# Optimization experiments

Hardware: AMD Instinct MI355X
Metric: run time of the kernel (lower is better)

The kernel has to match this reference:

```python
import jax, jax.numpy as jnp
import numpy as np

LN_EPS = 1e-3  # keras LayerNormalization default epsilon


def _prefix_weights(S, dtype):
    # W[i, j] = 1/(i-j)^2 for j < i, else 0  (distance = i - j)
    idx = jnp.arange(S)
    diff = idx[:, None] - idx[None, :]
    safe = jnp.where(diff > 0, diff, 1).astype(dtype)
    return jnp.where(diff > 0, 1.0 / (safe * safe), jnp.zeros((), dtype))


def setup_inputs() -> dict:
    key = jax.random.key(0)
    k1, k2 = jax.random.split(key)
    B, S, E = 2, 512, 256
    x = jax.random.normal(k1, (B, S, E), dtype=jnp.float32)
    concept_map = jax.random.normal(k2, (E, E, E), dtype=jnp.float32) * 0.02
    gamma = jnp.ones((E,), dtype=jnp.float32)
    beta = jnp.zeros((E,), dtype=jnp.float32)
    return {"x": x, "concept_map": concept_map, "gamma": gamma, "beta": beta}


def reference(x, concept_map, gamma, beta):
    B, S, E = x.shape
    # positional-weighted prefix sum: s[b,i,:] = sum_{j<i} x[b,j,:] / (i-j)^2
    W = _prefix_weights(S, x.dtype)            # (S, S) lower-triangular
    s = jnp.einsum('ij,bjd->bid', W, x)        # (B, S, E)
    # outer product x_i (x) s_i contracted with cubic concept_map:
    # result[b,i,c] = sum_{a,p} x[b,i,a] * s[b,i,p] * concept_map[c,a,p]
    # (stacked conceptual_matrices broadcast against concept_map, summed over
    #  the last two axes -- equivalent bilinear contraction)
    y = jnp.einsum('bsa,bsp,cap->bsc', x, s, concept_map)
    y = y + x  # residual
    # LayerNormalization over last axis (keras defaults: eps=1e-3, affine)
    mean = jnp.mean(y, axis=-1, keepdims=True)
    var = jnp.mean(jnp.square(y - mean), axis=-1, keepdims=True)
    y = (y - mean) * jax.lax.rsqrt(var + LN_EPS) * gamma + beta
    # Dropout is identity at inference
    return y
```

## Files before the change

### kernel.cpp

```cpp
#include <hip/hip_runtime.h>
#include <hip/hip_fp16.h>
#include <cstdint>

#define BB 2
#define SS 512
#define EE 256
#define NN (BB*SS)
#define KTOT (EE*EE)
#define SPLITK 32
#define KCHUNK (KTOT/SPLITK)
#define NSTEP (KCHUNK/32)
#define TSTEPS (KTOT/32)
#define LN_EPS 1e-3f

typedef _Float16 f16;
typedef _Float16 f16x8 __attribute__((ext_vector_type(8)));
typedef float    f32x4 __attribute__((ext_vector_type(4)));

#define NPACK 512

__global__ void prep_kernel(const float* __restrict__ cm, f16* __restrict__ cmP,
                            const float* __restrict__ x, float* __restrict__ ps) {
    __shared__ __align__(16) char smem[35072];
    const int bid = blockIdx.x;
    const int tid = threadIdx.x;
    const int wave = tid >> 6;
    const int lane = tid & 63;

    if (bid < NPACK) {
        const int cg = bid >> 7;
        const int kg = bid & 127;
        f16* lt = (f16*)smem;
        #pragma unroll
        for (int h = 0; h < 2; ++h) {
            #pragma unroll
            for (int i = 0; i < 8; ++i) {
                const int rl = i * 4 + wave;
                const int row = cg * 64 + h * 32 + rl;
                const float* src = cm + (size_t)row * KTOT + kg * 512 + lane * 8;
                float4 lo = *(const float4*)(src);
                float4 hi = *(const float4*)(src + 4);
                f16x8 v = { (f16)lo.x, (f16)lo.y, (f16)lo.z, (f16)lo.w,
                            (f16)hi.x, (f16)hi.y, (f16)hi.z, (f16)hi.w };
                *(f16x8*)(lt + lane * 264 + rl * 8) = v;
            }
            __syncthreads();
            #pragma unroll
            for (int jj = 0; jj < 8; ++jj) {
                const int s  = jj * 8 + wave * 2 + (lane >> 5);
                const int cl = lane & 31;
                f16x8 v = *(const f16x8*)(lt + s * 264 + cl * 8);
                const int t    = kg * 16 + (s >> 2);
                const int koct = s & 3;
                const int c    = cg * 64 + h * 32 + cl;
                *(f16x8*)(cmP + (size_t)t * 8192 + koct * 2048 + c * 8) = v;
            }
            __syncthreads();
        }
        return;
    }

    float (*xt)[128] = (float(*)[128])smem;
    float* wl2 = (float*)(smem + 32768);
    const int id = bid - NPACK;
    const int eh = id & 1;
    const int rest = id >> 1;
    const int b = rest / 36;
    const int r = rest % 36;
    int it = 0;
    while ((it + 1) * (it + 2) / 2 <= r) ++it;
    const int jt = r - it * (it + 1) / 2;

    for (int t = tid; t < 576; t += 256) {
        const int d = t - 64;
        wl2[t] = (d > 0) ? 1.0f / ((float)d * (float)d) : 0.0f;
    }
    const int jbase = jt * 64, ibase = it * 64;
    const float* xb = x + ((size_t)b * SS + jbase) * EE + eh * 128;
    #pragma unroll
    for (int p = 0; p < 8; ++p) {
        const int row = p * 8 + (tid >> 5);
        const int col = (tid & 31) * 4;
        *(float4*)&xt[row][col] = *(const float4*)(xb + (size_t)row * EE + col);
    }
    __syncthreads();

    const int g  = tid >> 5;
    const int ec = (tid & 31) * 4;
    const int irow = ibase + g * 8;
    float4 acc[8];
    #pragma unroll
    for (int m = 0; m < 8; ++m) acc[m] = (float4){0.f, 0.f, 0.f, 0.f};

    for (int jj = 0; jj < 64; ++jj) {
        const float4 xv = *(const float4*)&xt[jj][ec];
        const int wbase = irow - (jbase + jj) + 64;
        #pragma unroll
        for (int m = 0; m < 8; ++m) {
            const float w = wl2[wbase + m];
            acc[m].x += xv.x * w;
            acc[m].y += xv.y * w;
            acc[m].z += xv.z * w;
            acc[m].w += xv.w * w;
        }
    }

    float* base = ps + ((size_t)(((b * 2 + eh) * 8 + it) * 8 + jt)) * (64 * 128);
    #pragma unroll
    for (int m = 0; m < 8; ++m)
        *(float4*)(base + (size_t)(g * 8 + m) * 128 + ec) = acc[m];
}

__global__ void reduce_s_kernel(const float* __restrict__ ps, float* __restrict__ s) {
    const int n = blockIdx.x;
    const int e = threadIdx.x;
    const int b = n >> 9, i = n & (SS - 1);
    const int it = i >> 6, il = i & 63;
    const int eh = e >> 7, ec = e & 127;
    const size_t tbase = (size_t)((b * 2 + eh) * 8 + it) * 8;
    float acc = 0.0f;
    for (int jt = 0; jt <= it; ++jt)
        acc += ps[(tbase + jt) * (64 * 128) + (size_t)il * 128 + ec];
    s[(size_t)n * EE + e] = acc;
}

__launch_bounds__(256, 2)
__global__ void gemm_kernel(const float* __restrict__ x,
                            const float* __restrict__ sbuf,
                            const f16* __restrict__ cmP,
                            f16* __restrict__ part) {
    __shared__ __align__(16) f16 Ep[64 * 264];
    const int tid  = threadIdx.x;
    const int lane = tid & 63;
    const int wave = tid >> 6;
    const int koct = lane >> 4;
    const int cl   = lane & 15;

    const int d = blockIdx.x;
    const int nblock = (d >> 3) & 15;
    const int chunk  = (d & 7) * 4 + (d >> 7);

    f16x8 xf[4];
    #pragma unroll
    for (int rt = 0; rt < 4; ++rt) {
        const int r = nblock * 64 + rt * 16 + cl;
        const float* xr = x + (size_t)r * EE + chunk * 8;
        float4 xlo = *(const float4*)(xr);
        float4 xhi = *(const float4*)(xr + 4);
        xf[rt] = (f16x8){ (f16)xlo.x, (f16)xlo.y, (f16)xlo.z, (f16)xlo.w,
                          (f16)xhi.x, (f16)xhi.y, (f16)xhi.z, (f16)xhi.w };
    }
    float4 p0[4][2];
    #pragma unroll
    for (int rt = 0; rt < 4; ++rt) {
        const int r = nblock * 64 + rt * 16 + cl;
        const float* sr = sbuf + (size_t)r * EE + koct * 8;
        p0[rt][0] = *(const float4*)(sr);
        p0[rt][1] = *(const float4*)(sr + 4);
    }

    const char* bbase = (const char*)cmP + (size_t)chunk * (64 * 16384)
                      + koct * 4096 + wave * 1024 + cl * 16;
    #define TOFF(v) ((size_t)((((v) & 7) << 3) | ((v) >> 3)) * 16384)
    #define LOADB(BUF, v) do {                                              \
        _Pragma("unroll")                                                   \
        for (int ct_ = 0; ct_ < 4; ++ct_)                                   \
            BUF[ct_] = *(const f16x8*)(bbase + TOFF(v) + ct_ * 256);        \
    } while (0)

    f16x8 b0[4], b1[4], b2[4], b3[4];
    LOADB(b0, 0); LOADB(b1, 1); LOADB(b2, 2);
    __builtin_amdgcn_sched_barrier(0);

    f32x4 acc[4][4];
    #pragma unroll
    for (int a = 0; a < 4; ++a)
        #pragma unroll
        for (int b = 0; b < 4; ++b) acc[a][b] = (f32x4){0.f, 0.f, 0.f, 0.f};

    f16x8 svm[4];
    #pragma unroll
    for (int rt = 0; rt < 4; ++rt)
        svm[rt] = (f16x8){ (f16)p0[rt][0].x, (f16)p0[rt][0].y,
                           (f16)p0[rt][0].z, (f16)p0[rt][0].w,
                           (f16)p0[rt][1].x, (f16)p0[rt][1].y,
                           (f16)p0[rt][1].z, (f16)p0[rt][1].w };

    float4 pnxt[4][2];

    #define STEP(mm, aa, BU, BL) do {                                       \
        const int v_ = (mm) * 8 + (aa);                                     \
        if ((aa) == 6 && (mm) < 7) {                                        \
            _Pragma("unroll")                                               \
            for (int rt_ = 0; rt_ < 4; ++rt_) {                             \
                const int r_ = nblock * 64 + rt_ * 16 + cl;                 \
                const float* sr_ = sbuf + (size_t)r_ * EE + ((mm) + 1) * 32 \
                                 + koct * 8;                                \
                pnxt[rt_][0] = *(const float4*)(sr_);                       \
                pnxt[rt_][1] = *(const float4*)(sr_ + 4);                   \
            }                                                               \
        }                                                                   \
        f16x8 af_[4];                                                       \
        _Pragma("unroll")                                                   \
        for (int rt_ = 0; rt_ < 4; ++rt_) {                                 \
            const f16 xa_ = xf[rt_][(aa)];                                  \
            const f16x8 xa8_ = { xa_, xa_, xa_, xa_, xa_, xa_, xa_, xa_ };  \
            af_[rt_] = xa8_ * svm[rt_];                                     \
        }                                                                   \
        __builtin_amdgcn_s_setprio(1);                                      \
        _Pragma("unroll")                                                   \
        for (int ct_ = 0; ct_ < 4; ++ct_)                                   \
            _Pragma("unroll")                                               \
            for (int rt_ = 0; rt_ < 4; ++rt_)                               \
                acc[rt_][ct_] = __builtin_amdgcn_mfma_f32_16x16x32_f16(     \
                    af_[rt_], BU[ct_], acc[rt_][ct_], 0, 0, 0);             \
        __builtin_amdgcn_s_setprio(0);                                      \
        if (v_ + 3 < NSTEP) LOADB(BL, v_ + 3);                              \
        if ((aa) == 7 && (mm) < 7) {                                        \
            _Pragma("unroll")                                               \
            for (int rt_ = 0; rt_ < 4; ++rt_)                               \
                svm[rt_] = (f16x8){                                         \
                    (f16)pnxt[rt_][0].x, (f16)pnxt[rt_][0].y,               \
                    (f16)pnxt[rt_][0].z, (f16)pnxt[rt_][0].w,               \
                    (f16)pnxt[rt_][1].x, (f16)pnxt[rt_][1].y,               \
                    (f16)pnxt[rt_][1].z, (f16)pnxt[rt_][1].w };             \
        }                                                                   \
        __builtin_amdgcn_sched_barrier(0);                                  \
    } while (0)

    #pragma unroll
    for (int m = 0; m < 8; ++m) {
        STEP(m, 0, b0, b3);
        STEP(m, 1, b1, b0);
        STEP(m, 2, b2, b1);
        STEP(m, 3, b3, b2);
        STEP(m, 4, b0, b3);
        STEP(m, 5, b1, b0);
        STEP(m, 6, b2, b1);
        STEP(m, 7, b3, b2);
    }
    #undef STEP
    #undef LOADB
    #undef TOFF

    __syncthreads();
    #pragma unroll
    for (int rt = 0; rt < 4; ++rt) {
        #pragma unroll
        for (int ct = 0; ct < 4; ++ct) {
            const int col = wave * 64 + ct * 16 + cl;
            #pragma unroll
            for (int q = 0; q < 4; ++q) {
                const int lr = rt * 16 + koct * 4 + q;
                Ep[lr * 264 + col] = (f16)acc[rt][ct][q];
            }
        }
    }
    __syncthreads();
    {
        const int lr  = tid >> 2;
        const int seg = tid & 3;
        f16* dst = part + ((size_t)chunk * NN + nblock * 64 + lr) * EE + seg * 64;
        const f16* srcE = Ep + lr * 264 + seg * 64;
        #pragma unroll
        for (int i = 0; i < 8; ++i)
            *(f16x8*)(dst + i * 8) = *(const f16x8*)(srcE + i * 8);
    }
}

__global__ void reduce_ln_kernel(const float* __restrict__ x,
                                 const f16* __restrict__ part,
                                 const float* __restrict__ gamma,
                                 const float* __restrict__ beta,
                                 float* __restrict__ out) {
    const int n = blockIdx.x;
    const int c = threadIdx.x;
    const int lane = c & 63, wave = c >> 6;
    float y = x[(size_t)n * EE + c];
    #pragma unroll 8
    for (int ch = 0; ch < SPLITK; ++ch)
        y += (float)part[((size_t)ch * NN + n) * EE + c];

    float v = y;
    #pragma unroll
    for (int o = 32; o > 0; o >>= 1) v += __shfl_xor(v, o);
    __shared__ float red[8];
    if (lane == 0) red[wave] = v;
    __syncthreads();
    const float mean = (red[0] + red[1] + red[2] + red[3]) * (1.0f / EE);
    const float d = y - mean;
    float sq = d * d;
    #pragma unroll
    for (int o = 32; o > 0; o >>= 1) sq += __shfl_xor(sq, o);
    if (lane == 0) red[4 + wave] = sq;
    __syncthreads();
    const float var = (red[4] + red[5] + red[6] + red[7]) * (1.0f / EE);
    out[(size_t)n * EE + c] = d * rsqrtf(var + LN_EPS) * gamma[c] + beta[c];
}

extern "C" void kernel_launch(void* const* d_in, const int* in_sizes, int n_in,
                              void* d_out, int out_size, void* d_ws, size_t ws_size,
                              hipStream_t stream) {
    const float* x     = (const float*)d_in[0];
    const float* cm    = (const float*)d_in[1];
    const float* gamma = (const float*)d_in[2];
    const float* beta  = (const float*)d_in[3];
    float* out = (float*)d_out;

    float* sbuf = (float*)d_ws;
    f16*   cmP  = (f16*)(sbuf + (size_t)NN * EE);
    f16*   part = (f16*)((char*)cmP + (size_t)TSTEPS * 8192 * sizeof(f16));
    float* ps   = (float*)part;

    hipLaunchKernelGGL(prep_kernel, dim3(NPACK + 144), dim3(256), 0, stream,
                       cm, cmP, x, ps);
    hipLaunchKernelGGL(reduce_s_kernel, dim3(NN), dim3(256), 0, stream, ps, sbuf);
    hipLaunchKernelGGL(gemm_kernel, dim3(16 * SPLITK), dim3(256), 0, stream,
                       x, sbuf, cmP, part);
    hipLaunchKernelGGL(reduce_ln_kernel, dim3(NN), dim3(256), 0, stream,
                       x, part, gamma, beta, out);
}
```

Before: 72.34 us.

## Accumulate prefix-sum tiles in-block and drop the separate s reduction kernel

The weighted prefix sum is now computed by 32 blocks, each looping over all preceding j-tiles and writing s directly. This replaces 144 partial-tile blocks plus a reduce_s_kernel launch, removing a launch and the partial-buffer round trip. The cost is a more imbalanced, serial tail: the last row-tile block runs 8 tiles while the pack blocks finish. The sched_barrier hints in the GEMM main loop are also removed, handing instruction scheduling back to the compiler.

```diff
diff --git a/kernel.cpp b/kernel.cpp
--- a/kernel.cpp
+++ b/kernel.cpp
@@ -9,7 +9,7 @@
 #define KTOT (EE*EE)
 #define SPLITK 32
 #define KCHUNK (KTOT/SPLITK)
-#define NSTEP (KCHUNK/32)
+#define NSTEP 64
 #define TSTEPS (KTOT/32)
 #define LN_EPS 1e-3f
 
@@ -20,7 +20,7 @@
 #define NPACK 512
 
 __global__ void prep_kernel(const float* __restrict__ cm, f16* __restrict__ cmP,
-                            const float* __restrict__ x, float* __restrict__ ps) {
+                            const float* __restrict__ x, float* __restrict__ s) {
     __shared__ __align__(16) char smem[35072];
     const int bid = blockIdx.x;
     const int tid = threadIdx.x;
@@ -47,11 +47,11 @@
             __syncthreads();
             #pragma unroll
             for (int jj = 0; jj < 8; ++jj) {
-                const int s  = jj * 8 + wave * 2 + (lane >> 5);
+                const int sl = jj * 8 + wave * 2 + (lane >> 5);
                 const int cl = lane & 31;
-                f16x8 v = *(const f16x8*)(lt + s * 264 + cl * 8);
-                const int t    = kg * 16 + (s >> 2);
-                const int koct = s & 3;
+                f16x8 v = *(const f16x8*)(lt + sl * 264 + cl * 8);
+                const int t    = kg * 16 + (sl >> 2);
+                const int koct = sl & 3;
                 const int c    = cg * 64 + h * 32 + cl;
                 *(f16x8*)(cmP + (size_t)t * 8192 + koct * 2048 + c * 8) = v;
             }
@@ -64,26 +64,14 @@
     float* wl2 = (float*)(smem + 32768);
     const int id = bid - NPACK;
     const int eh = id & 1;
-    const int rest = id >> 1;
-    const int b = rest / 36;
-    const int r = rest % 36;
-    int it = 0;
-    while ((it + 1) * (it + 2) / 2 <= r) ++it;
-    const int jt = r - it * (it + 1) / 2;
+    const int b  = (id >> 1) & 1;
+    const int it = id >> 2;
+    const int ibase = it * 64;
 
     for (int t = tid; t < 576; t += 256) {
         const int d = t - 64;
         wl2[t] = (d > 0) ? 1.0f / ((float)d * (float)d) : 0.0f;
     }
-    const int jbase = jt * 64, ibase = it * 64;
-    const float* xb = x + ((size_t)b * SS + jbase) * EE + eh * 128;
-    #pragma unroll
-    for (int p = 0; p < 8; ++p) {
-        const int row = p * 8 + (tid >> 5);
-        const int col = (tid & 31) * 4;
-        *(float4*)&xt[row][col] = *(const float4*)(xb + (size_t)row * EE + col);
-    }
-    __syncthreads();
 
     const int g  = tid >> 5;
     const int ec = (tid & 31) * 4;
@@ -92,36 +80,35 @@
     #pragma unroll
     for (int m = 0; m < 8; ++m) acc[m] = (float4){0.f, 0.f, 0.f, 0.f};
 
-    for (int jj = 0; jj < 64; ++jj) {
-        const float4 xv = *(const float4*)&xt[jj][ec];
-        const int wbase = irow - (jbase + jj) + 64;
-        #pragma unroll
-        for (int m = 0; m < 8; ++m) {
-            const float w = wl2[wbase + m];
-            acc[m].x += xv.x * w;
-            acc[m].y += xv.y * w;
-            acc[m].z += xv.z * w;
-            acc[m].w += xv.w * w;
+    for (int jt = 0; jt <= it; ++jt) {
+        const int jbase = jt * 64;
+        __syncthreads();
+        const float* xb = x + ((size_t)b * SS + jbase) * EE + eh * 128;
+        #pragma unroll
+        for (int p = 0; p < 8; ++p) {
+            const int row = p * 8 + (tid >> 5);
+            const int col = (tid & 31) * 4;
+            *(float4*)&xt[row][col] = *(const float4*)(xb + (size_t)row * EE + col);
         }
-    }
-
-    float* base = ps + ((size_t)(((b * 2 + eh) * 8 + it) * 8 + jt)) * (64 * 128);
+        __syncthreads();
+        for (int jj = 0; jj < 64; ++jj) {
+            const float4 xv = *(const float4*)&xt[jj][ec];
+            const int wbase = irow - (jbase + jj) + 64;
+            #pragma unroll
+            for (int m = 0; m < 8; ++m) {
+                const float w = wl2[wbase + m];
+                acc[m].x += xv.x * w;
+                acc[m].y += xv.y * w;
+                acc[m].z += xv.z * w;
+                acc[m].w += xv.w * w;
+            }
+        }
+    }
+
+    float* base = s + ((size_t)b * SS + ibase) * EE + eh * 128;
     #pragma unroll
     for (int m = 0; m < 8; ++m)
-        *(float4*)(base + (size_t)(g * 8 + m) * 128 + ec) = acc[m];
-}
-
-__global__ void reduce_s_kernel(const float* __restrict__ ps, float* __restrict__ s) {
-    const int n = blockIdx.x;
-    const int e = threadIdx.x;
-    const int b = n >> 9, i = n & (SS - 1);
-    const int it = i >> 6, il = i & 63;
-    const int eh = e >> 7, ec = e & 127;
-    const size_t tbase = (size_t)((b * 2 + eh) * 8 + it) * 8;
-    float acc = 0.0f;
-    for (int jt = 0; jt <= it; ++jt)
-        acc += ps[(tbase + jt) * (64 * 128) + (size_t)il * 128 + ec];
-    s[(size_t)n * EE + e] = acc;
+        *(float4*)(base + (size_t)(g * 8 + m) * EE + ec) = acc[m];
 }
 
 __launch_bounds__(256, 2)
@@ -170,7 +157,6 @@
 
     f16x8 b0[4], b1[4], b2[4], b3[4];
     LOADB(b0, 0); LOADB(b1, 1); LOADB(b2, 2);
-    __builtin_amdgcn_sched_barrier(0);
 
     f32x4 acc[4][4];
     #pragma unroll
@@ -225,7 +211,6 @@
                     (f16)pnxt[rt_][1].x, (f16)pnxt[rt_][1].y,               \
                     (f16)pnxt[rt_][1].z, (f16)pnxt[rt_][1].w };             \
         }                                                                   \
-        __builtin_amdgcn_sched_barrier(0);                                  \
     } while (0)
 
     #pragma unroll
@@ -310,11 +295,9 @@
     float* sbuf = (float*)d_ws;
     f16*   cmP  = (f16*)(sbuf + (size_t)NN * EE);
     f16*   part = (f16*)((char*)cmP + (size_t)TSTEPS * 8192 * sizeof(f16));
-    float* ps   = (float*)part;
-
-    hipLaunchKernelGGL(prep_kernel, dim3(NPACK + 144), dim3(256), 0, stream,
-                       cm, cmP, x, ps);
-    hipLaunchKernelGGL(reduce_s_kernel, dim3(NN), dim3(256), 0, stream, ps, sbuf);
+
+    hipLaunchKernelGGL(prep_kernel, dim3(NPACK + 32), dim3(256), 0, stream,
+                       cm, cmP, x, sbuf);
     hipLaunchKernelGGL(gemm_kernel, dim3(16 * SPLITK), dim3(256), 0, stream,
                        x, sbuf, cmP, part);
     hipLaunchKernelGGL(reduce_ln_kernel, dim3(NN), dim3(256), 0, stream,
```

Measured after the change: 92.99 us. +28.5%, slower.
